# Performance work log

Measured on AMD Instinct MI355X. Metric: run time of the kernel, lower is better.

Reference implementation:

```python
import jax, jax.numpy as jnp
import numpy as np

D_MODEL = 1024
NUM_HEADS = 16
DEPTH = D_MODEL // NUM_HEADS


def setup_inputs() -> dict:
    key = jax.random.key(0)
    ks = jax.random.split(key, 13)
    B, S = 4, 2048
    s = 1.0 / np.sqrt(D_MODEL)
    return {
        "query": jax.random.normal(ks[0], (B, S, D_MODEL), jnp.float32),
        "key": jax.random.normal(ks[1], (B, S, D_MODEL), jnp.float32),
        "value": jax.random.normal(ks[2], (B, S, D_MODEL), jnp.float32),
        "mask": jax.random.uniform(ks[3], (B, 1, 1, S), jnp.float32),
        "Wq": jax.random.normal(ks[4], (D_MODEL, D_MODEL), jnp.float32) * s,
        "bq": jnp.zeros((D_MODEL,), jnp.float32),
        "Wk": jax.random.normal(ks[5], (D_MODEL, D_MODEL), jnp.float32) * s,
        "bk": jnp.zeros((D_MODEL,), jnp.float32),
        "Wv": jax.random.normal(ks[6], (D_MODEL, D_MODEL), jnp.float32) * s,
        "bv": jnp.zeros((D_MODEL,), jnp.float32),
        "Wo": jax.random.normal(ks[7], (D_MODEL, D_MODEL), jnp.float32) * s,
        "bo": jnp.zeros((D_MODEL,), jnp.float32),
    }


def _split_heads(x):
    # [B, S, d_model] -> [B, H, S, depth]
    B, S, _ = x.shape
    return x.reshape(B, S, NUM_HEADS, DEPTH).transpose(0, 2, 1, 3)


def reference(query, key, value, mask, Wq, bq, Wk, bk, Wv, bv, Wo, bo):
    q = _split_heads(query @ Wq + bq)   # [B,H,Sq,dh]
    k = _split_heads(key @ Wk + bk)     # [B,H,Sk,dh]
    v = _split_heads(value @ Wv + bv)   # [B,H,Sk,dh]
    scale = 1.0 / jnp.sqrt(jnp.float32(DEPTH))
    scores = jnp.einsum("bhqd,bhkd->bhqk", q, k) * scale
    scores = scores + mask * -1e9
    attn = jax.nn.softmax(scores, axis=-1)
    out = jnp.einsum("bhqk,bhkd->bhqd", attn, v)  # [B,H,Sq,dh]
    B, _, Sq, _ = out.shape
    concat = out.transpose(0, 2, 1, 3).reshape(B, Sq, D_MODEL)
    return concat @ Wo + bo
```

## Files before the change

kernel.cpp:

```cpp
#include <hip/hip_runtime.h>

typedef unsigned short ushort_t;
typedef __attribute__((ext_vector_type(8))) short short8;
typedef __attribute__((ext_vector_type(4))) float f32x4;
typedef __attribute__((ext_vector_type(16))) float f32x16;
typedef __attribute__((ext_vector_type(2))) unsigned int uint2v;
typedef __attribute__((ext_vector_type(4))) unsigned int uint4v;
typedef __attribute__((ext_vector_type(2))) unsigned int uint2s;

typedef __attribute__((address_space(1))) const unsigned char gaddr_t;
typedef __attribute__((address_space(3))) unsigned char laddr_t;

__device__ __forceinline__ unsigned short f2bf(float x) {
  unsigned u = __float_as_uint(x);
  u += 0x7FFF + ((u >> 16) & 1);
  return (unsigned short)(u >> 16);
}
__device__ __forceinline__ float bf2f(unsigned short u) {
  return __uint_as_float(((unsigned)u) << 16);
}
__device__ __forceinline__ unsigned cvt_pk_bf16(float lo, float hi) {
  unsigned r;
  asm("v_cvt_pk_bf16_f32 %0, %1, %2" : "=v"(r) : "v"(lo), "v"(hi));
  return r;
}

__device__ __forceinline__ void gl_lds16(const void* g, void* l) {
  __builtin_amdgcn_global_load_lds((gaddr_t*)g, (laddr_t*)l, 16, 0, 0);
}

__device__ __forceinline__ unsigned active_mask(const float* __restrict__ tb) {
  unsigned am = 0;
  float run = -INFINITY;
#pragma unroll
  for (int tt = 0; tt < 32; tt++) {
    float tm = tb[tt];
    if (tm > run - 40.f) am |= (1u << tt);
    run = fmaxf(run, tm);
  }
  return am;
}

__global__ void prep0(const float* __restrict__ maskin, float* __restrict__ maskpre,
                      float* __restrict__ tmaxbuf) {
  const float CM = -1.442695041e9f;
  int bx = blockIdx.x;
  if (bx < 8) {
    int i = bx * 1024 + threadIdx.x * 4;
    f32x4 v = *(const f32x4*)(maskin + i);
    v *= CM;
    *(f32x4*)(maskpre + i) = v;
  } else {
    int t = threadIdx.x;
    if (t < 128) {
      const float* src = maskin + (t >> 5) * 2048 + (t & 31) * 64;
      float mn = src[0];
#pragma unroll
      for (int j = 1; j < 64; j++) mn = fminf(mn, src[j]);
      tmaxbuf[t] = mn * CM;
    }
  }
}

__global__ void prep1(const float4* __restrict__ q4, const float4* __restrict__ k4,
                      const float4* __restrict__ v4,
                      ushort4* __restrict__ xq, ushort4* __restrict__ xk,
                      ushort4* __restrict__ xv,
                      const float* __restrict__ W0, const float* __restrict__ W1,
                      const float* __restrict__ W2, const float* __restrict__ W3,
                      ushort_t* __restrict__ T0, ushort_t* __restrict__ T1,
                      ushort_t* __restrict__ T2, ushort_t* __restrict__ T3,
                      const float* __restrict__ tmaxbuf) {
  const int K = 1024, N = 1024;
  __shared__ ushort_t tile[32][33];
  int bx = blockIdx.x;
  if (bx < 3072) {
    int z = bx >> 10, bl = bx & 1023;
    if (z > 0) {
      int b = bl >> 8, tl = (bl >> 3) & 31;
      unsigned am = active_mask(tmaxbuf + b * 32);
      if (!((am >> tl) & 1u)) return;
    }
    const float4* in = (z == 0) ? q4 : (z == 1) ? k4 : v4;
    ushort4* out = (z == 0) ? xq : (z == 1) ? xk : xv;
    const float4* src = in + (long)bl * 2048;
    ushort4* dst = out + (long)bl * 2048;
    int t = threadIdx.x;
#pragma unroll
    for (int j = 0; j < 8; j++) {
      int idx = j * 256 + t;
      float4 v = src[idx];
      ushort4 o;
      o.x = f2bf(v.x); o.y = f2bf(v.y); o.z = f2bf(v.z); o.w = f2bf(v.w);
      dst[idx] = o;
    }
  } else {
    int idx = bx - 3072;
    int z = idx >> 10;
    const float* W = (z == 0) ? W0 : (z == 1) ? W1 : (z == 2) ? W2 : W3;
    ushort_t* Wt = (z == 0) ? T0 : (z == 1) ? T1 : (z == 2) ? T2 : T3;
    int n0 = (idx & 31) * 32, k0 = ((idx >> 5) & 31) * 32;
    int tx = threadIdx.x & 31, ty = threadIdx.x >> 5;
#pragma unroll
    for (int r = 0; r < 4; r++) {
      int k = k0 + ty + r * 8;
      tile[ty + r * 8][tx] = f2bf(W[(long)k * N + n0 + tx]);
    }
    __syncthreads();
#pragma unroll
    for (int r = 0; r < 4; r++) {
      int n = n0 + ty + r * 8;
      Wt[(long)n * K + k0 + tx] = tile[tx][ty + r * 8];
    }
  }
}

__global__ void gemm_qkv3(
    const ushort_t* __restrict__ Aq, const ushort_t* __restrict__ Ak, const ushort_t* __restrict__ Av,
    const ushort_t* __restrict__ Bq, const ushort_t* __restrict__ Bk, const ushort_t* __restrict__ Bv,
    const float* __restrict__ bq, const float* __restrict__ bk, const float* __restrict__ bv,
    ushort_t* __restrict__ Cq, ushort_t* __restrict__ Ck, ushort_t* __restrict__ Vt,
    const float* __restrict__ tmaxbuf) {
  const int K = 1024, N = 1024;
  const int z = blockIdx.z;
  const ushort_t* A = z == 0 ? Aq : z == 1 ? Ak : Av;
  const ushort_t* Bt = z == 0 ? Bq : z == 1 ? Bk : Bv;
  const float* bias = z == 0 ? bq : z == 1 ? bk : bv;

  __shared__ __align__(16) char smem[32768];
  const int t = threadIdx.x, w = t >> 6, l = t & 63;

  const int orig = blockIdx.x + gridDim.x * blockIdx.y;
  const int xcd = orig & 7, i = orig >> 3;
  const int m0 = (xcd * 8 + (i & 7)) * 128;
  const int n0 = (i >> 3) * 128;
  const int wr = (w >> 1) * 64, wc = (w & 1) * 64;

  if (z != 0) {
    int b_ = m0 >> 11, tile0 = (m0 & 2047) >> 6;
    unsigned am = active_mask(tmaxbuf + b_ * 32);
    if (!((am >> tile0) & 3u)) return;
  }

  f32x4 acc[4][4] = {};

  const int o0 = w * 1024 + l * 16;
  const int br0 = o0 >> 6, bc0 = (o0 & 63) >> 1;
  const int o1 = 4096 + o0;
  const int br1 = o1 >> 6, bc1 = (o1 & 63) >> 1;
  const ushort_t* Ab = A + (long)m0 * K;
  const ushort_t* Bb = Bt + (long)n0 * K;

  auto stage = [&](int kk, int buf) {
    gl_lds16(Ab + (long)br0 * K + kk + bc0, smem + buf * 8192 + w * 1024);
    gl_lds16(Ab + (long)br1 * K + kk + bc1, smem + buf * 8192 + 4096 + w * 1024);
    gl_lds16(Bb + (long)br0 * K + kk + bc0, smem + 16384 + buf * 8192 + w * 1024);
    gl_lds16(Bb + (long)br1 * K + kk + bc1, smem + 16384 + buf * 8192 + 4096 + w * 1024);
  };

  stage(0, 0);
  __syncthreads();

  for (int ts = 0; ts < 32; ts++) {
    const int cur = ts & 1;
    if (ts < 31) stage((ts + 1) * 32, cur ^ 1);

    const ushort_t* Asb = (const ushort_t*)(smem + cur * 8192);
    const ushort_t* Bsb = (const ushort_t*)(smem + 16384 + cur * 8192);
    short8 af[4], bfr[4];
#pragma unroll
    for (int m = 0; m < 4; m++)
      af[m] = *(const short8*)&Asb[(wr + m * 16 + (l & 15)) * 32 + ((l >> 4) * 8)];
#pragma unroll
    for (int n = 0; n < 4; n++)
      bfr[n] = *(const short8*)&Bsb[(wc + n * 16 + (l & 15)) * 32 + ((l >> 4) * 8)];
    __builtin_amdgcn_s_setprio(1);
#pragma unroll
    for (int m = 0; m < 4; m++)
#pragma unroll
      for (int n = 0; n < 4; n++)
        acc[m][n] = __builtin_amdgcn_mfma_f32_16x16x32_bf16(af[m], bfr[n], acc[m][n], 0, 0, 0);
    __builtin_amdgcn_s_setprio(0);
    __syncthreads();
  }

  char* Lw = smem + w * 8192;
  if (z != 2) {
#pragma unroll
    for (int nn = 0; nn < 4; nn++) {
      float bvv = bias[n0 + wc + nn * 16 + (l & 15)];
      int dl = nn * 16 + (l & 15);
#pragma unroll
      for (int mm = 0; mm < 4; mm++)
#pragma unroll
        for (int i2 = 0; i2 < 4; i2++) {
          int sl = mm * 16 + (l >> 4) * 4 + i2;
          *(ushort_t*)(Lw + sl * 128 + ((dl * 2) ^ ((sl & 7) << 4))) =
              f2bf(acc[mm][nn][i2] + bvv);
        }
    }
    ushort_t* C = (z == 0 ? Cq : Ck) + (long)(m0 + wr) * N + n0 + wc;
#pragma unroll
    for (int rr = 0; rr < 8; rr++) {
      int sl = rr * 8 + (l >> 3);
      short8 vv = *(const short8*)(Lw + sl * 128 + (((l & 7) * 16) ^ ((sl & 7) << 4)));
      *(short8*)(C + (long)sl * N + (l & 7) * 8) = vv;
    }
  } else {
#pragma unroll
    for (int nn = 0; nn < 4; nn++) {
      float bvv = bias[n0 + wc + nn * 16 + (l & 15)];
      int dl = nn * 16 + (l & 15);
#pragma unroll
      for (int mm = 0; mm < 4; mm++) {
        int sl = mm * 16 + (l >> 4) * 4;
        uint2s pk;
        pk.x = cvt_pk_bf16(acc[mm][nn][0] + bvv, acc[mm][nn][1] + bvv);
        pk.y = cvt_pk_bf16(acc[mm][nn][2] + bvv, acc[mm][nn][3] + bvv);
        *(uint2s*)(Lw + dl * 128 + ((sl * 2) ^ ((dl & 7) << 4))) = pk;
      }
    }
    const int b_ = m0 >> 11;
    const int s0g = (m0 & 2047) + wr;
#pragma unroll
    for (int rr = 0; rr < 8; rr++) {
      int dl = rr * 8 + (l >> 3);
      short8 vv = *(const short8*)(Lw + dl * 128 + (((l & 7) * 16) ^ ((dl & 7) << 4)));
      int dg = n0 + wc + dl;
      long rowbase = ((long)(b_ * 16 + (dg >> 6)) * 64 + (dg & 63)) * 2048;
      *(short8*)(Vt + rowbase + s0g + (l & 7) * 8) = vv;
    }
  }
}

__global__ void gemm_o(const ushort_t* __restrict__ A, const ushort_t* __restrict__ Bt,
                       const float* __restrict__ bias, float* __restrict__ C) {
  const int K = 1024, N = 1024;
  __shared__ __align__(16) ushort_t As[2][128 * 32];
  __shared__ __align__(16) ushort_t Bs[2][128 * 32];
  const int t = threadIdx.x, w = t >> 6, l = t & 63;

  const int orig = blockIdx.x + gridDim.x * blockIdx.y;
  const int xcd = orig & 7, i = orig >> 3;
  const int m0 = (xcd * 8 + (i & 7)) * 128;
  const int n0 = (i >> 3) * 128;
  const int wr = (w >> 1) * 64, wc = (w & 1) * 64;

  f32x4 acc[4][4] = {};

  const int o0 = w * 1024 + l * 16;
  const int br0 = o0 >> 6, bc0 = (o0 & 63) >> 1;
  const int o1 = 4096 + o0;
  const int br1 = o1 >> 6, bc1 = (o1 & 63) >> 1;
  const ushort_t* Ab = A + (long)m0 * K;
  const ushort_t* Bb = Bt + (long)n0 * K;

  auto stage = [&](int kk, int buf) {
    gl_lds16(Ab + (long)br0 * K + kk + bc0, (char*)&As[buf][0] + w * 1024);
    gl_lds16(Ab + (long)br1 * K + kk + bc1, (char*)&As[buf][0] + 4096 + w * 1024);
    gl_lds16(Bb + (long)br0 * K + kk + bc0, (char*)&Bs[buf][0] + w * 1024);
    gl_lds16(Bb + (long)br1 * K + kk + bc1, (char*)&Bs[buf][0] + 4096 + w * 1024);
  };

  stage(0, 0);
  __syncthreads();

  for (int ts = 0; ts < 32; ts++) {
    const int cur = ts & 1;
    if (ts < 31) stage((ts + 1) * 32, cur ^ 1);

    short8 af[4], bfr[4];
#pragma unroll
    for (int m = 0; m < 4; m++)
      af[m] = *(const short8*)&As[cur][(wr + m * 16 + (l & 15)) * 32 + ((l >> 4) * 8)];
#pragma unroll
    for (int n = 0; n < 4; n++)
      bfr[n] = *(const short8*)&Bs[cur][(wc + n * 16 + (l & 15)) * 32 + ((l >> 4) * 8)];
    __builtin_amdgcn_s_setprio(1);
#pragma unroll
    for (int m = 0; m < 4; m++)
#pragma unroll
      for (int n = 0; n < 4; n++)
        acc[m][n] = __builtin_amdgcn_mfma_f32_16x16x32_bf16(af[m], bfr[n], acc[m][n], 0, 0, 0);
    __builtin_amdgcn_s_setprio(0);
    __syncthreads();
  }

#pragma unroll
  for (int mm = 0; mm < 4; mm++)
#pragma unroll
    for (int nn = 0; nn < 4; nn++) {
      int c = n0 + wc + nn * 16 + (l & 15);
      float bv = bias[c];
#pragma unroll
      for (int i2 = 0; i2 < 4; i2++) {
        int r = m0 + wr + mm * 16 + (l >> 4) * 4 + i2;
        C[(long)r * N + c] = acc[mm][nn][i2] + bv;
      }
    }
}

__global__ __launch_bounds__(256, 4) void attn(
    const ushort_t* __restrict__ Qp, const ushort_t* __restrict__ Kp,
    const ushort_t* __restrict__ Vt, const float* __restrict__ maskpre,
    const float* __restrict__ tmaxbuf, ushort_t* __restrict__ Ob) {
  const int S = 2048, DM = 1024;
  __shared__ __align__(16) char smem[32768];
  char* KlB = smem;
  char* VlB = smem + 16384;

  const int t = threadIdx.x, w = t >> 6, l = t & 63;
  const int lq = l & 31, hi = l >> 5;
  const int hib = hi * 16;

  const int orig = blockIdx.x + (blockIdx.y << 4) + (blockIdx.z << 8);
  const int work = ((orig & 7) << 7) + (orig >> 3);
  const int qx = work & 15;
  const int hb = work >> 4;
  const int h = hb & 15, b = hb >> 4;
  const int q0w = qx * 128 + w * 32;

  const float C1 = 0.1803368801f;

  const ushort_t* Kbase = Kp + (long)(b * S) * DM + h * 64;
  const ushort_t* Vbase = Vt + (long)((b * 16 + h) * 64) * S;
  const float* Mbase = maskpre + (long)b * S;

  short8 qB[4];
  {
    const ushort_t* Qb = Qp + ((long)(b * S) + q0w + lq) * DM + h * 64;
#pragma unroll
    for (int kh = 0; kh < 4; kh++)
      qB[kh] = *(const short8*)(Qb + kh * 16 + hi * 8);
  }

  const int so0 = w * 2048 + l * 16;
  const int sr0 = so0 >> 7, sc0 = (so0 & 127) ^ ((sr0 & 7) << 4);
  const int so1 = so0 + 1024;
  const int sr1 = so1 >> 7, sc1 = (so1 & 127) ^ ((sr1 & 7) << 4);
  const ushort_t* Kg0 = Kbase + (long)sr0 * DM + (sc0 >> 1);
  const ushort_t* Kg1 = Kbase + (long)sr1 * DM + (sc1 >> 1);
  const ushort_t* Vg0 = Vbase + (long)sr0 * S + (sc0 >> 1);
  const ushort_t* Vg1 = Vbase + (long)sr1 * S + (sc1 >> 1);
  char* Kd0 = KlB + w * 2048;
  char* Vd0 = VlB + w * 2048;

  auto stage = [&](int kv0, int bb) {
    long ko = (long)kv0 * DM;
    int bo = bb * 8192;
    gl_lds16(Kg0 + ko, Kd0 + bo);
    gl_lds16(Kg1 + ko, Kd0 + bo + 1024);
    gl_lds16(Vg0 + kv0, Vd0 + bo);
    gl_lds16(Vg1 + kv0, Vd0 + bo + 1024);
  };

  unsigned amask = active_mask(tmaxbuf + b * 32);

  int cur = (int)__builtin_ctz(amask);
  stage(cur * 64, 0);
  __syncthreads();

  const int lbase = lq * 128 + ((lq & 7) << 4);

  f32x16 o0 = {}, o1 = {};
  float mrun = -INFINITY, lsum = 0.f;
  int bb = 0;

  while (cur >= 0) {
    unsigned rem = amask & (0xFFFFFFFEu << cur);
    int nxt = rem ? (int)__builtin_ctz(rem) : -1;
    if (nxt >= 0) stage(nxt * 64, bb ^ 1);
    const int bx = lbase + (bb << 13);
    const int kv0 = cur * 64;

    f32x16 s0 = {}, s1 = {};
    __builtin_amdgcn_s_setprio(1);
#pragma unroll
    for (int kh = 0; kh < 4; kh++) {
      int a = bx ^ (kh * 32 + hib);
      short8 ka0 = *(const short8*)(KlB + a);
      short8 ka1 = *(const short8*)(KlB + a + 4096);
      s0 = __builtin_amdgcn_mfma_f32_32x32x16_bf16(ka0, qB[kh], s0, 0, 0, 0);
      s1 = __builtin_amdgcn_mfma_f32_32x32x16_bf16(ka1, qB[kh], s1, 0, 0, 0);
    }
    __builtin_amdgcn_s_setprio(0);

    const float* mq = Mbase + kv0;
#pragma unroll
    for (int g = 0; g < 4; g++) {
      f32x4 m0 = *(const f32x4*)(mq + g * 8 + hi * 4);
      f32x4 m1 = *(const f32x4*)(mq + 32 + g * 8 + hi * 4);
#pragma unroll
      for (int c = 0; c < 4; c++) {
        s0[g * 4 + c] = fmaf(s0[g * 4 + c], C1, m0[c]);
        s1[g * 4 + c] = fmaf(s1[g * 4 + c], C1, m1[c]);
      }
    }

    float mx0 = -INFINITY, mx1 = -INFINITY, mx2 = -INFINITY, mx3 = -INFINITY;
#pragma unroll
    for (int r = 0; r < 4; r++) {
      mx0 = fmaxf(mx0, fmaxf(s0[r], s0[r + 4]));
      mx1 = fmaxf(mx1, fmaxf(s0[r + 8], s0[r + 12]));
      mx2 = fmaxf(mx2, fmaxf(s1[r], s1[r + 4]));
      mx3 = fmaxf(mx3, fmaxf(s1[r + 8], s1[r + 12]));
    }
    float mx = fmaxf(fmaxf(mx0, mx1), fmaxf(mx2, mx3));
    mx = fmaxf(mx, __shfl_xor(mx, 32));

    if (!__all((int)(mx <= mrun + 8.f))) {
      float mnew = fmaxf(mrun, mx);
      float sc = __builtin_amdgcn_exp2f(mrun - mnew);
      mrun = mnew;
      lsum *= sc;
#pragma unroll
      for (int r = 0; r < 16; r++) { o0[r] *= sc; o1[r] *= sc; }
    }

    float ps0 = 0.f, ps1 = 0.f, ps2 = 0.f, ps3 = 0.f;
#pragma unroll
    for (int r = 0; r < 8; r++) {
      float p0 = __builtin_amdgcn_exp2f(s0[r] - mrun);
      float p1 = __builtin_amdgcn_exp2f(s0[r + 8] - mrun);
      float p2 = __builtin_amdgcn_exp2f(s1[r] - mrun);
      float p3 = __builtin_amdgcn_exp2f(s1[r + 8] - mrun);
      s0[r] = p0; s0[r + 8] = p1; s1[r] = p2; s1[r + 8] = p3;
      ps0 += p0; ps1 += p1; ps2 += p2; ps3 += p3;
    }
    float ps = (ps0 + ps1) + (ps2 + ps3);
    ps += __shfl_xor(ps, 32);
    lsum += ps;

#pragma unroll
    for (int half = 0; half < 2; half++) {
      const f32x16& sv = half ? s1 : s0;
      unsigned x0 = cvt_pk_bf16(sv[0], sv[1]);
      unsigned z0 = cvt_pk_bf16(sv[2], sv[3]);
      unsigned y0 = cvt_pk_bf16(sv[4], sv[5]);
      unsigned u0 = cvt_pk_bf16(sv[6], sv[7]);
      unsigned x1 = cvt_pk_bf16(sv[8], sv[9]);
      unsigned z1 = cvt_pk_bf16(sv[10], sv[11]);
      unsigned y1 = cvt_pk_bf16(sv[12], sv[13]);
      unsigned u1 = cvt_pk_bf16(sv[14], sv[15]);
      uint2v a1 = __builtin_amdgcn_permlane32_swap(x0, y0, false, false);
      uint2v a2 = __builtin_amdgcn_permlane32_swap(z0, u0, false, false);
      uint2v a3 = __builtin_amdgcn_permlane32_swap(x1, y1, false, false);
      uint2v a4 = __builtin_amdgcn_permlane32_swap(z1, u1, false, false);
      uint4v f0, f1;
      f0.x = a1.x; f0.y = a2.x; f0.z = a1.y; f0.w = a2.y;
      f1.x = a3.x; f1.y = a4.x; f1.z = a3.y; f1.w = a4.y;
      short8 pB0 = __builtin_bit_cast(short8, f0);
      short8 pB1 = __builtin_bit_cast(short8, f1);
      __builtin_amdgcn_s_setprio(1);
#pragma unroll
      for (int kt2 = 0; kt2 < 2; kt2++) {
        short8 pB = kt2 ? pB1 : pB0;
        int a = bx ^ (half * 64 + kt2 * 32 + hib);
        short8 va0 = *(const short8*)(VlB + a);
        short8 va1 = *(const short8*)(VlB + a + 4096);
        o0 = __builtin_amdgcn_mfma_f32_32x32x16_bf16(va0, pB, o0, 0, 0, 0);
        o1 = __builtin_amdgcn_mfma_f32_32x32x16_bf16(va1, pB, o1, 0, 0, 0);
      }
      __builtin_amdgcn_s_setprio(0);
    }
    __syncthreads();
    bb ^= 1;
    cur = nxt;
  }

  __syncthreads();
  char* Ow = smem + w * 4096;
  float inv = 1.0f / lsum;
#pragma unroll
  for (int r = 0; r < 16; r++) {
    int d0 = (r & 3) + 8 * (r >> 2) + 4 * hi;
    int a0 = lq * 128 + ((d0 * 2) ^ ((lq & 7) << 4));
    *(ushort_t*)(Ow + a0) = f2bf(o0[r] * inv);
    int d1 = 32 + d0;
    int a1 = lq * 128 + ((d1 * 2) ^ ((lq & 7) << 4));
    *(ushort_t*)(Ow + a1) = f2bf(o1[r] * inv);
  }
  ushort_t* Obase = Ob + ((long)(b * S) + q0w) * DM + h * 64;
#pragma unroll
  for (int rr = 0; rr < 4; rr++) {
    int q = rr * 8 + (l >> 3);
    int a = q * 128 + (((l & 7) * 16) ^ ((q & 7) << 4));
    short8 vv = *(const short8*)(Ow + a);
    *(short8*)(Obase + (long)q * DM + (l & 7) * 8) = vv;
  }
}

extern "C" void kernel_launch(void* const* d_in, const int* in_sizes, int n_in,
                              void* d_out, int out_size, void* d_ws, size_t ws_size,
                              hipStream_t stream) {
  const float* query = (const float*)d_in[0];
  const float* key   = (const float*)d_in[1];
  const float* value = (const float*)d_in[2];
  const float* mask  = (const float*)d_in[3];
  const float* Wq = (const float*)d_in[4];
  const float* bq = (const float*)d_in[5];
  const float* Wk = (const float*)d_in[6];
  const float* bk = (const float*)d_in[7];
  const float* Wv = (const float*)d_in[8];
  const float* bv = (const float*)d_in[9];
  const float* Wo = (const float*)d_in[10];
  const float* bo = (const float*)d_in[11];

  const int B = 4, S = 2048, DM = 1024, H = 16;
  const long M = (long)B * S;
  const long XB = (long)1 << 24;

  char* ws = (char*)d_ws;
  ushort_t* Wqt = (ushort_t*)(ws);
  ushort_t* Wkt = (ushort_t*)(ws + (1l << 21));
  ushort_t* Wvt = (ushort_t*)(ws + 2 * (1l << 21));
  ushort_t* Wot = (ushort_t*)(ws + 3 * (1l << 21));
  ushort_t* Xv  = (ushort_t*)(ws + 4 * (1l << 21));
  ushort_t* Qp  = (ushort_t*)(ws + 4 * (1l << 21) + XB);
  ushort_t* Kp  = Qp + M * DM;
  ushort_t* Vtr = Kp + M * DM;
  float* maskpre = (float*)(Vtr + M * DM);
  float* tmaxbuf = maskpre + (long)B * S;
  ushort_t* AO  = Xv;
  ushort_t* Xq  = (ushort_t*)d_out;
  ushort_t* Xk  = Xq + M * DM;

  prep0<<<9, 256, 0, stream>>>(mask, maskpre, tmaxbuf);

  prep1<<<7168, 256, 0, stream>>>((const float4*)query, (const float4*)key,
                                  (const float4*)value, (ushort4*)Xq, (ushort4*)Xk,
                                  (ushort4*)Xv, Wq, Wk, Wv, Wo, Wqt, Wkt, Wvt, Wot,
                                  tmaxbuf);

  gemm_qkv3<<<dim3(64, 8, 3), 256, 0, stream>>>(Xq, Xk, Xv, Wqt, Wkt, Wvt,
                                                bq, bk, bv, Qp, Kp, Vtr, tmaxbuf);

  attn<<<dim3(16, 16, 4), 256, 0, stream>>>(Qp, Kp, Vtr, maskpre, tmaxbuf, AO);

  gemm_o<<<dim3(64, 8), 256, 0, stream>>>(AO, Wot, bo, (float*)d_out);
}
```

Before: 131.9 us.

## Triple-buffer GEMM LDS staging with swizzled layout and partial vmcnt waits

Both projection GEMMs (QKV and output) move from double to triple-buffered LDS staging. Global-to-LDS loads are issued two k-steps ahead, and the loop waits only on older loads via vmcnt(4) plus a raw s_barrier instead of a full __syncthreads. The staging layout also gains an XOR swizzle on load columns and fragment reads to reduce LDS bank conflicts. This costs 48KB of LDS per block, which may lower occupancy, and the hand-placed waitcnt logic is fragile.

```diff
diff --git a/kernel.cpp b/kernel.cpp
--- a/kernel.cpp
+++ b/kernel.cpp
@@ -127,7 +127,7 @@
   const ushort_t* Bt = z == 0 ? Bq : z == 1 ? Bk : Bv;
   const float* bias = z == 0 ? bq : z == 1 ? bk : bv;
 
-  __shared__ __align__(16) char smem[32768];
+  __shared__ __align__(16) char smem[49152];
   const int t = threadIdx.x, w = t >> 6, l = t & 63;
 
   const int orig = blockIdx.x + gridDim.x * blockIdx.y;
@@ -144,36 +144,40 @@
 
   f32x4 acc[4][4] = {};
 
-  const int o0 = w * 1024 + l * 16;
-  const int br0 = o0 >> 6, bc0 = (o0 & 63) >> 1;
-  const int o1 = 4096 + o0;
-  const int br1 = o1 >> 6, bc1 = (o1 & 63) >> 1;
+  const int br0 = 16 * w + (l >> 2);
+  const int bcs = ((l & 3) ^ ((l >> 3) & 3)) << 3;
   const ushort_t* Ab = A + (long)m0 * K;
   const ushort_t* Bb = Bt + (long)n0 * K;
 
   auto stage = [&](int kk, int buf) {
-    gl_lds16(Ab + (long)br0 * K + kk + bc0, smem + buf * 8192 + w * 1024);
-    gl_lds16(Ab + (long)br1 * K + kk + bc1, smem + buf * 8192 + 4096 + w * 1024);
-    gl_lds16(Bb + (long)br0 * K + kk + bc0, smem + 16384 + buf * 8192 + w * 1024);
-    gl_lds16(Bb + (long)br1 * K + kk + bc1, smem + 16384 + buf * 8192 + 4096 + w * 1024);
+    char* base = smem + buf * 16384;
+    gl_lds16(Ab + (long)br0 * K + kk + bcs, base + w * 1024);
+    gl_lds16(Ab + (long)(br0 + 64) * K + kk + bcs, base + 4096 + w * 1024);
+    gl_lds16(Bb + (long)br0 * K + kk + bcs, base + 8192 + w * 1024);
+    gl_lds16(Bb + (long)(br0 + 64) * K + kk + bcs, base + 12288 + w * 1024);
   };
 
   stage(0, 0);
-  __syncthreads();
+  stage(32, 1);
+
+  const int fsw = ((l >> 4) ^ ((l >> 1) & 3)) << 4;
+  const int arow = (wr + (l & 15)) * 64 + fsw;
+  const int brow = 8192 + (wc + (l & 15)) * 64 + fsw;
+
+  asm volatile("s_waitcnt vmcnt(4)");
+  __builtin_amdgcn_sched_barrier(0);
+  __builtin_amdgcn_s_barrier();
 
   for (int ts = 0; ts < 32; ts++) {
-    const int cur = ts & 1;
-    if (ts < 31) stage((ts + 1) * 32, cur ^ 1);
-
-    const ushort_t* Asb = (const ushort_t*)(smem + cur * 8192);
-    const ushort_t* Bsb = (const ushort_t*)(smem + 16384 + cur * 8192);
+    const char* base = smem + (ts % 3) * 16384;
+    if (ts + 2 < 32) stage((ts + 2) * 32, (ts + 2) % 3);
     short8 af[4], bfr[4];
 #pragma unroll
     for (int m = 0; m < 4; m++)
-      af[m] = *(const short8*)&Asb[(wr + m * 16 + (l & 15)) * 32 + ((l >> 4) * 8)];
+      af[m] = *(const short8*)(base + arow + m * 1024);
 #pragma unroll
     for (int n = 0; n < 4; n++)
-      bfr[n] = *(const short8*)&Bsb[(wc + n * 16 + (l & 15)) * 32 + ((l >> 4) * 8)];
+      bfr[n] = *(const short8*)(base + brow + n * 1024);
     __builtin_amdgcn_s_setprio(1);
 #pragma unroll
     for (int m = 0; m < 4; m++)
@@ -181,8 +185,14 @@
       for (int n = 0; n < 4; n++)
         acc[m][n] = __builtin_amdgcn_mfma_f32_16x16x32_bf16(af[m], bfr[n], acc[m][n], 0, 0, 0);
     __builtin_amdgcn_s_setprio(0);
-    __syncthreads();
-  }
+    if (ts < 30) asm volatile("s_waitcnt vmcnt(4)");
+    else if (ts == 30) asm volatile("s_waitcnt vmcnt(0)");
+    if (ts < 31) {
+      __builtin_amdgcn_sched_barrier(0);
+      __builtin_amdgcn_s_barrier();
+    }
+  }
+  __builtin_amdgcn_s_barrier();
 
   char* Lw = smem + w * 8192;
   if (z != 2) {
@@ -236,8 +246,7 @@
 __global__ void gemm_o(const ushort_t* __restrict__ A, const ushort_t* __restrict__ Bt,
                        const float* __restrict__ bias, float* __restrict__ C) {
   const int K = 1024, N = 1024;
-  __shared__ __align__(16) ushort_t As[2][128 * 32];
-  __shared__ __align__(16) ushort_t Bs[2][128 * 32];
+  __shared__ __align__(16) char smem[49152];
   const int t = threadIdx.x, w = t >> 6, l = t & 63;
 
   const int orig = blockIdx.x + gridDim.x * blockIdx.y;
@@ -248,34 +257,40 @@
 
   f32x4 acc[4][4] = {};
 
-  const int o0 = w * 1024 + l * 16;
-  const int br0 = o0 >> 6, bc0 = (o0 & 63) >> 1;
-  const int o1 = 4096 + o0;
-  const int br1 = o1 >> 6, bc1 = (o1 & 63) >> 1;
+  const int br0 = 16 * w + (l >> 2);
+  const int bcs = ((l & 3) ^ ((l >> 3) & 3)) << 3;
   const ushort_t* Ab = A + (long)m0 * K;
   const ushort_t* Bb = Bt + (long)n0 * K;
 
   auto stage = [&](int kk, int buf) {
-    gl_lds16(Ab + (long)br0 * K + kk + bc0, (char*)&As[buf][0] + w * 1024);
-    gl_lds16(Ab + (long)br1 * K + kk + bc1, (char*)&As[buf][0] + 4096 + w * 1024);
-    gl_lds16(Bb + (long)br0 * K + kk + bc0, (char*)&Bs[buf][0] + w * 1024);
-    gl_lds16(Bb + (long)br1 * K + kk + bc1, (char*)&Bs[buf][0] + 4096 + w * 1024);
+    char* base = smem + buf * 16384;
+    gl_lds16(Ab + (long)br0 * K + kk + bcs, base + w * 1024);
+    gl_lds16(Ab + (long)(br0 + 64) * K + kk + bcs, base + 4096 + w * 1024);
+    gl_lds16(Bb + (long)br0 * K + kk + bcs, base + 8192 + w * 1024);
+    gl_lds16(Bb + (long)(br0 + 64) * K + kk + bcs, base + 12288 + w * 1024);
   };
 
   stage(0, 0);
-  __syncthreads();
+  stage(32, 1);
+
+  const int fsw = ((l >> 4) ^ ((l >> 1) & 3)) << 4;
+  const int arow = (wr + (l & 15)) * 64 + fsw;
+  const int brow = 8192 + (wc + (l & 15)) * 64 + fsw;
+
+  asm volatile("s_waitcnt vmcnt(4)");
+  __builtin_amdgcn_sched_barrier(0);
+  __builtin_amdgcn_s_barrier();
 
   for (int ts = 0; ts < 32; ts++) {
-    const int cur = ts & 1;
-    if (ts < 31) stage((ts + 1) * 32, cur ^ 1);
-
+    const char* base = smem + (ts % 3) * 16384;
+    if (ts + 2 < 32) stage((ts + 2) * 32, (ts + 2) % 3);
     short8 af[4], bfr[4];
 #pragma unroll
     for (int m = 0; m < 4; m++)
-      af[m] = *(const short8*)&As[cur][(wr + m * 16 + (l & 15)) * 32 + ((l >> 4) * 8)];
+      af[m] = *(const short8*)(base + arow + m * 1024);
 #pragma unroll
     for (int n = 0; n < 4; n++)
-      bfr[n] = *(const short8*)&Bs[cur][(wc + n * 16 + (l & 15)) * 32 + ((l >> 4) * 8)];
+      bfr[n] = *(const short8*)(base + brow + n * 1024);
     __builtin_amdgcn_s_setprio(1);
 #pragma unroll
     for (int m = 0; m < 4; m++)
@@ -283,7 +298,12 @@
       for (int n = 0; n < 4; n++)
         acc[m][n] = __builtin_amdgcn_mfma_f32_16x16x32_bf16(af[m], bfr[n], acc[m][n], 0, 0, 0);
     __builtin_amdgcn_s_setprio(0);
-    __syncthreads();
+    if (ts < 30) asm volatile("s_waitcnt vmcnt(4)");
+    else if (ts == 30) asm volatile("s_waitcnt vmcnt(0)");
+    if (ts < 31) {
+      __builtin_amdgcn_sched_barrier(0);
+      __builtin_amdgcn_s_barrier();
+    }
   }
 
 #pragma unroll
```

Result: no change. 130.5 us, median of 4 (-1.1%).
